# Optimization experiments

Measured on AMD Instinct MI355X. Metric: run time of the kernel, lower is better.

Reference implementation:

```python
import jax, jax.numpy as jnp
import numpy as np

IMAGE_SIZE = 256
NUM_FACES = 4096
NEAR = 0.1
FAR = 100.0
DRAW_BACKSIDE = False
EPS = 1e-8
CHUNK = 128  # faces processed per scan step (memory/compute tradeoff)


def setup_inputs() -> dict:
    key = jax.random.key(0)
    u = jax.random.uniform(key, (1, NUM_FACES, 3, 3), dtype=jnp.float32)  # fill=rand
    xy = u[..., :2] * 2.0 - 1.0          # screen coords in [-1, 1]
    z = u[..., 2:] * 20.0 + 1.0          # depths in [1, 21], inside (near, far)
    # shrink triangles toward their centroid -> realistic small screen-space triangles
    center = jnp.mean(xy, axis=2, keepdims=True)
    xy = center + (xy - center) * 0.15
    faces = jnp.concatenate([xy, z], axis=-1)  # [B, F, 3, 3]
    return {"faces": faces}


def _rasterize(faces):
    """Z-buffer triangle rasterization. Returns (depth_map, face_index_map).
    Matches the CUDA 'safe' kernel: per pixel, loop faces; point-in-triangle via
    same-sign edge functions; perspective-correct depth 1/zp = sum(w_i / z_i);
    keep the closest face with zp in (near, far); -1 where nothing is drawn.
    Faces are scanned in chunks to avoid materializing [B, F, S, S]."""
    B, F = faces.shape[0], faces.shape[1]
    S = IMAGE_SIZE
    ax = jnp.arange(S, dtype=jnp.float32)
    # pixel centers in normalized coords: p = (2*i + 1 - S) / S
    yp = (2.0 * ax + 1.0 - S) / S
    xp = (2.0 * ax + 1.0 - S) / S
    YP = yp[None, None, :, None]   # [1,1,S,1]
    XP = xp[None, None, None, :]   # [1,1,1,S]

    n_chunks = F // CHUNK
    fc = faces.reshape(B, n_chunks, CHUNK, 3, 3).transpose(1, 0, 2, 3, 4)  # [n,B,C,3,3]
    bases = jnp.arange(n_chunks, dtype=jnp.int32) * CHUNK

    def body(carry, inp):
        best_depth, best_face = carry          # [B,S,S] each
        fchunk, base = inp                     # [B,C,3,3], scalar face offset
        def vtx(k, c):
            return fchunk[:, :, k, c][..., None, None]  # [B,C,1,1]
        x0, y0, z0 = vtx(0, 0), vtx(0, 1), vtx(0, 2)
        x1, y1, z1 = vtx(1, 0), vtx(1, 1), vtx(1, 2)
        x2, y2, z2 = vtx(2, 0), vtx(2, 1), vtx(2, 2)

        # edge functions (unnormalized barycentric weights), [B,C,S,S]
        w0 = (YP - y1) * (x2 - x1) - (XP - x1) * (y2 - y1)
        w1 = (YP - y2) * (x0 - x2) - (XP - x2) * (y0 - y2)
        w2 = (YP - y0) * (x1 - x0) - (XP - x0) * (y1 - y0)
        inside = (w0 * w1 > 0) & (w1 * w2 > 0)  # strictly same sign -> inside

        w_sum = w0 + w1 + w2                    # sign encodes winding order
        facing = jnp.ones_like(inside) if DRAW_BACKSIDE else (w_sum > 0)

        # perspective-correct depth: zp = 1 / sum((w_i / w_sum) / z_i)
        denom = w0 / z0 + w1 / z1 + w2 / z2
        denom = jnp.where(jnp.abs(denom) > EPS, denom, EPS)
        zp = w_sum / denom

        valid = inside & facing & (NEAR < zp) & (zp < FAR)
        depth = jnp.where(valid, zp, FAR)       # [B,C,S,S]

        chunk_depth = jnp.min(depth, axis=1)            # [B,S,S]
        chunk_idx = jnp.argmin(depth, axis=1)
        update = chunk_depth < best_depth               # strict '<' like the CUDA loop
        best_depth = jnp.where(update, chunk_depth, best_depth)
        best_face = jnp.where(update, (base + chunk_idx).astype(jnp.int32), best_face)
        return (best_depth, best_face), None

    init = (jnp.full((B, S, S), FAR, jnp.float32),
            jnp.full((B, S, S), -1, jnp.int32))
    (best_depth, best_face), _ = jax.lax.scan(body, init, (fc, bases))
    return best_depth, best_face


def reference(faces):
    _, face_index_map = _rasterize(faces)
    return face_index_map  # [B, S, S] int32, -1 where no face covers the pixel
```

## Files before the change

### kernel.cpp

```cpp
#include <hip/hip_runtime.h>

#define S 256
#define NF 4096
#define TILE 16
#define NT 1024
#define SLICES 4
#define CAP 1024
#define NEARF 0.1f
#define FARF 100.0f
#define EPSF 1e-8f

__global__ __launch_bounds__(NT) void raster_tile(const float* __restrict__ faces,
                                                  int* __restrict__ out) {
    __shared__ float4 s_data[CAP][3];
    __shared__ int s_ids[NF];
    __shared__ unsigned long long s_key[NT];
    __shared__ int s_count;

    const int tile = blockIdx.x;
    const int tx0 = (tile & (S / TILE - 1)) * TILE;
    const int ty0 = (tile / (S / TILE)) * TILE;

    if (threadIdx.x == 0) s_count = 0;
    __syncthreads();

    const float cxlo = (2.0f * tx0 + 1.0f - 256.0f) * (1.0f / 256.0f) - 1e-5f;
    const float cxhi = (2.0f * (tx0 + TILE - 1) + 1.0f - 256.0f) * (1.0f / 256.0f) + 1e-5f;
    const float cylo = (2.0f * ty0 + 1.0f - 256.0f) * (1.0f / 256.0f) - 1e-5f;
    const float cyhi = (2.0f * (ty0 + TILE - 1) + 1.0f - 256.0f) * (1.0f / 256.0f) + 1e-5f;

    for (int f = threadIdx.x; f < NF; f += NT) {
        const float* p = faces + f * 9;
        const float x0 = p[0], y0 = p[1], z0 = p[2];
        const float x1 = p[3], y1 = p[4], z1 = p[5];
        const float x2 = p[6], y2 = p[7], z2 = p[8];
        const float bxmin = fminf(x0, fminf(x1, x2));
        const float bxmax = fmaxf(x0, fmaxf(x1, x2));
        const float bymin = fminf(y0, fminf(y1, y2));
        const float bymax = fmaxf(y0, fmaxf(y1, y2));
        bool hit = (bxmax >= cxlo) && (bxmin <= cxhi) && (bymax >= cylo) && (bymin <= cyhi);
        if (hit) {
            const double a2 = ((double)x1 - (double)x0) * ((double)y2 - (double)y0) -
                              ((double)x2 - (double)x0) * ((double)y1 - (double)y0);
            hit = (a2 > -1e-4);
        }
        if (hit) {
            const int pos = atomicAdd(&s_count, 1);
            s_ids[pos] = f;
            if (pos < CAP) {
                s_data[pos][0] = make_float4(x0, y0, x1, y1);
                s_data[pos][1] = make_float4(x2, y2, z0, z1);
                s_data[pos][2] = make_float4(z2, __int_as_float(f), 0.0f, 0.0f);
            }
        }
    }
    __syncthreads();
    const int n = s_count;
    const int nc = n < CAP ? n : CAP;

    const int pix = threadIdx.x & 255;
    const int slice = threadIdx.x >> 8;
    const int px = tx0 + (pix & (TILE - 1));
    const int py = ty0 + (pix / TILE);
    const float xp = (2.0f * px + 1.0f - 256.0f) * (1.0f / 256.0f);
    const float yp = (2.0f * py + 1.0f - 256.0f) * (1.0f / 256.0f);

    float bestd = FARF;
    int bestf = 0x7fffffff;

#define BODY(X0, Y0, Z0, X1, Y1, Z1, X2, Y2, Z2, FIDX)                                   \
    {                                                                                    \
        const float w0 = __fsub_rn(__fmul_rn(__fsub_rn(yp, Y1), __fsub_rn(X2, X1)),      \
                                   __fmul_rn(__fsub_rn(xp, X1), __fsub_rn(Y2, Y1)));     \
        const float w1 = __fsub_rn(__fmul_rn(__fsub_rn(yp, Y2), __fsub_rn(X0, X2)),      \
                                   __fmul_rn(__fsub_rn(xp, X2), __fsub_rn(Y0, Y2)));     \
        const float w2 = __fsub_rn(__fmul_rn(__fsub_rn(yp, Y0), __fsub_rn(X1, X0)),      \
                                   __fmul_rn(__fsub_rn(xp, X0), __fsub_rn(Y1, Y0)));     \
        const bool inside = (__fmul_rn(w0, w1) > 0.0f) && (__fmul_rn(w1, w2) > 0.0f);    \
        const float wsum = __fadd_rn(__fadd_rn(w0, w1), w2);                             \
        if (inside && (wsum > 0.0f)) {                                                   \
            float denom = __fadd_rn(__fadd_rn(__fdiv_rn(w0, Z0), __fdiv_rn(w1, Z1)),     \
                                    __fdiv_rn(w2, Z2));                                  \
            denom = (fabsf(denom) > EPSF) ? denom : EPSF;                                \
            const float zp = __fdiv_rn(wsum, denom);                                     \
            if ((zp > NEARF) && (zp < FARF)) {                                           \
                if (zp < bestd || (zp == bestd && (FIDX) < bestf)) {                     \
                    bestd = zp;                                                          \
                    bestf = (FIDX);                                                      \
                }                                                                        \
            }                                                                            \
        }                                                                                \
    }

    for (int i = slice; i < nc; i += SLICES) {
        const float4 d0 = s_data[i][0];
        const float4 d1 = s_data[i][1];
        const float4 d2 = s_data[i][2];
        const int f = __float_as_int(d2.y);
        BODY(d0.x, d0.y, d1.z, d0.z, d0.w, d1.w, d1.x, d1.y, d2.x, f)
    }
    for (int i = CAP + slice; i < n; i += SLICES) {
        const int f = s_ids[i];
        const float* p = faces + f * 9;
        BODY(p[0], p[1], p[2], p[3], p[4], p[5], p[6], p[7], p[8], f)
    }
#undef BODY

    s_key[threadIdx.x] =
        ((unsigned long long)__float_as_uint(bestd) << 32) | (unsigned int)bestf;
    __syncthreads();
    if (threadIdx.x < 256) {
        unsigned long long k = s_key[threadIdx.x];
        unsigned long long k1 = s_key[threadIdx.x + 256];
        unsigned long long k2 = s_key[threadIdx.x + 512];
        unsigned long long k3 = s_key[threadIdx.x + 768];
        k = k1 < k ? k1 : k;
        k = k2 < k ? k2 : k;
        k = k3 < k ? k3 : k;
        const float d = __uint_as_float((unsigned int)(k >> 32));
        const int fi = (int)(unsigned int)k;
        const int opx = tx0 + (threadIdx.x & (TILE - 1));
        const int opy = ty0 + (threadIdx.x / TILE);
        out[opy * S + opx] = (d < FARF) ? fi : -1;
    }
}

extern "C" void kernel_launch(void* const* d_in, const int* in_sizes, int n_in,
                              void* d_out, int out_size, void* d_ws, size_t ws_size,
                              hipStream_t stream) {
    const float* faces = (const float*)d_in[0];
    int* out = (int*)d_out;
    hipLaunchKernelGGL(raster_tile, dim3((S / TILE) * (S / TILE)), dim3(NT), 0, stream,
                       faces, out);
}
```

Before: 30.12 us.

## Stage faces in shared-memory chunks with coalesced float4 loads before per-tile binning

```diff
diff --git a/kernel.cpp b/kernel.cpp
--- a/kernel.cpp
+++ b/kernel.cpp
@@ -5,58 +5,25 @@
 #define TILE 16
 #define NT 1024
 #define SLICES 4
-#define CAP 1024
+#define CHUNKF 1024
+#define NCHUNK (NF / CHUNKF)
+#define CAPC 256
 #define NEARF 0.1f
 #define FARF 100.0f
 #define EPSF 1e-8f
 
 __global__ __launch_bounds__(NT) void raster_tile(const float* __restrict__ faces,
                                                   int* __restrict__ out) {
-    __shared__ float4 s_data[CAP][3];
-    __shared__ int s_ids[NF];
+    __shared__ float4 s_face[CHUNKF * 9 / 4];
+    __shared__ float4 s_cand[CAPC][3];
     __shared__ unsigned long long s_key[NT];
-    __shared__ int s_count;
+    __shared__ int s_cnt;
+
+    const float* s_face_f = (const float*)s_face;
 
     const int tile = blockIdx.x;
     const int tx0 = (tile & (S / TILE - 1)) * TILE;
     const int ty0 = (tile / (S / TILE)) * TILE;
-
-    if (threadIdx.x == 0) s_count = 0;
-    __syncthreads();
-
-    const float cxlo = (2.0f * tx0 + 1.0f - 256.0f) * (1.0f / 256.0f) - 1e-5f;
-    const float cxhi = (2.0f * (tx0 + TILE - 1) + 1.0f - 256.0f) * (1.0f / 256.0f) + 1e-5f;
-    const float cylo = (2.0f * ty0 + 1.0f - 256.0f) * (1.0f / 256.0f) - 1e-5f;
-    const float cyhi = (2.0f * (ty0 + TILE - 1) + 1.0f - 256.0f) * (1.0f / 256.0f) + 1e-5f;
-
-    for (int f = threadIdx.x; f < NF; f += NT) {
-        const float* p = faces + f * 9;
-        const float x0 = p[0], y0 = p[1], z0 = p[2];
-        const float x1 = p[3], y1 = p[4], z1 = p[5];
-        const float x2 = p[6], y2 = p[7], z2 = p[8];
-        const float bxmin = fminf(x0, fminf(x1, x2));
-        const float bxmax = fmaxf(x0, fmaxf(x1, x2));
-        const float bymin = fminf(y0, fminf(y1, y2));
-        const float bymax = fmaxf(y0, fmaxf(y1, y2));
-        bool hit = (bxmax >= cxlo) && (bxmin <= cxhi) && (bymax >= cylo) && (bymin <= cyhi);
-        if (hit) {
-            const double a2 = ((double)x1 - (double)x0) * ((double)y2 - (double)y0) -
-                              ((double)x2 - (double)x0) * ((double)y1 - (double)y0);
-            hit = (a2 > -1e-4);
-        }
-        if (hit) {
-            const int pos = atomicAdd(&s_count, 1);
-            s_ids[pos] = f;
-            if (pos < CAP) {
-                s_data[pos][0] = make_float4(x0, y0, x1, y1);
-                s_data[pos][1] = make_float4(x2, y2, z0, z1);
-                s_data[pos][2] = make_float4(z2, __int_as_float(f), 0.0f, 0.0f);
-            }
-        }
-    }
-    __syncthreads();
-    const int n = s_count;
-    const int nc = n < CAP ? n : CAP;
 
     const int pix = threadIdx.x & 255;
     const int slice = threadIdx.x >> 8;
@@ -64,6 +31,11 @@
     const int py = ty0 + (pix / TILE);
     const float xp = (2.0f * px + 1.0f - 256.0f) * (1.0f / 256.0f);
     const float yp = (2.0f * py + 1.0f - 256.0f) * (1.0f / 256.0f);
+
+    const float cxlo = (2.0f * tx0 + 1.0f - 256.0f) * (1.0f / 256.0f) - 1e-5f;
+    const float cxhi = (2.0f * (tx0 + TILE - 1) + 1.0f - 256.0f) * (1.0f / 256.0f) + 1e-5f;
+    const float cylo = (2.0f * ty0 + 1.0f - 256.0f) * (1.0f / 256.0f) - 1e-5f;
+    const float cyhi = (2.0f * (ty0 + TILE - 1) + 1.0f - 256.0f) * (1.0f / 256.0f) + 1e-5f;
 
     float bestd = FARF;
     int bestf = 0x7fffffff;
@@ -92,17 +64,58 @@
         }                                                                                \
     }
 
-    for (int i = slice; i < nc; i += SLICES) {
-        const float4 d0 = s_data[i][0];
-        const float4 d1 = s_data[i][1];
-        const float4 d2 = s_data[i][2];
-        const int f = __float_as_int(d2.y);
-        BODY(d0.x, d0.y, d1.z, d0.z, d0.w, d1.w, d1.x, d1.y, d2.x, f)
-    }
-    for (int i = CAP + slice; i < n; i += SLICES) {
-        const int f = s_ids[i];
-        const float* p = faces + f * 9;
-        BODY(p[0], p[1], p[2], p[3], p[4], p[5], p[6], p[7], p[8], f)
+    for (int c = 0; c < NCHUNK; ++c) {
+        __syncthreads();
+
+        const float4* gsrc = (const float4*)faces + (size_t)c * (CHUNKF * 9 / 4);
+        for (int k = threadIdx.x; k < CHUNKF * 9 / 4; k += NT)
+            s_face[k] = gsrc[k];
+        if (threadIdx.x == 0) s_cnt = 0;
+        __syncthreads();
+
+        {
+            const float* p = s_face_f + threadIdx.x * 9;
+            const float x0 = p[0], y0 = p[1], z0 = p[2];
+            const float x1 = p[3], y1 = p[4], z1 = p[5];
+            const float x2 = p[6], y2 = p[7], z2 = p[8];
+            const float bxmin = fminf(x0, fminf(x1, x2));
+            const float bxmax = fmaxf(x0, fmaxf(x1, x2));
+            const float bymin = fminf(y0, fminf(y1, y2));
+            const float bymax = fmaxf(y0, fmaxf(y1, y2));
+            bool hit = (bxmax >= cxlo) && (bxmin <= cxhi) &&
+                       (bymax >= cylo) && (bymin <= cyhi);
+            if (hit) {
+                const double a2 = ((double)x1 - (double)x0) * ((double)y2 - (double)y0) -
+                                  ((double)x2 - (double)x0) * ((double)y1 - (double)y0);
+                hit = (a2 > -1e-4);
+            }
+            if (hit) {
+                const int slot = atomicAdd(&s_cnt, 1);
+                if (slot < CAPC) {
+                    s_cand[slot][0] = make_float4(x0, y0, x1, y1);
+                    s_cand[slot][1] = make_float4(x2, y2, z0, z1);
+                    s_cand[slot][2] =
+                        make_float4(z2, __int_as_float(c * CHUNKF + threadIdx.x), 0.0f, 0.0f);
+                }
+            }
+        }
+        __syncthreads();
+
+        const int n = s_cnt;
+        if (n <= CAPC) {
+            for (int i = slice; i < n; i += SLICES) {
+                const float4 d0 = s_cand[i][0];
+                const float4 d1 = s_cand[i][1];
+                const float4 d2 = s_cand[i][2];
+                const int f = __float_as_int(d2.y);
+                BODY(d0.x, d0.y, d1.z, d0.z, d0.w, d1.w, d1.x, d1.y, d2.x, f)
+            }
+        } else {
+            for (int i = slice; i < CHUNKF; i += SLICES) {
+                const float* p = s_face_f + i * 9;
+                BODY(p[0], p[1], p[2], p[3], p[4], p[5], p[6], p[7], p[8], c * CHUNKF + i)
+            }
+        }
     }
 #undef BODY
 
```

Result: slower. 33.56 us (+11.4%).
